# Performance work log

Measured on AMD Instinct MI355X. Metric: run time of the kernel, lower is better.

The kernel has to match this reference:

```python
import jax, jax.numpy as jnp
import numpy as np
from functools import partial

NP = 1024      # particles
T = 128        # timesteps
CUR_MIN, CUR_MAX = -2.0, 4.0
E_CRIT = 29000.0
F_STD = 0.005
G_STD = 0.01
NU = 1.0 / (G_STD * np.sqrt(2.0 * np.pi))

# VoC battery open-circuit-voltage curve constants
V_L, V_0 = -1.59614486, 4.13646328
GAMMA, ALPHA, BETA = 0.63726463, 1.40174122, 2.54478965


def voc(soc):
    return (V_L + (V_0 - V_L) * jnp.exp(GAMMA * (soc - 1.0))
            + ALPHA * V_L * (soc - 1.0)
            + (1.0 - ALPHA) * V_L * (jnp.exp(-BETA) - jnp.exp(-BETA * jnp.sqrt(soc))))


def setup_inputs() -> dict:
    key = jax.random.key(0)
    ks = jax.random.split(key, 11)
    soc_init = jax.random.uniform(ks[0], (NP, 1), jnp.float32, 0.3, 1.0)
    current = jax.random.normal(ks[1], (1, T), jnp.float32) * 0.5 + 1.0
    voltage_measured = 3.7 + 0.1 * jax.random.normal(ks[2], (1, T), jnp.float32)
    W1 = jax.random.normal(ks[3], (2, 1024), jnp.float32) / np.sqrt(2.0)
    b1 = jnp.zeros((1024,), jnp.float32)
    W2 = jax.random.normal(ks[4], (1024, 512), jnp.float32) / np.sqrt(1024.0)
    b2 = jnp.zeros((512,), jnp.float32)
    W3 = jax.random.normal(ks[5], (512, 1), jnp.float32) / np.sqrt(512.0)
    b3 = jnp.zeros((1,), jnp.float32)
    noise = jax.random.normal(ks[6], (T, NP, 1), jnp.float32)  # unit-std process noise
    u = jax.random.uniform(ks[7], (T,), jnp.float32)           # systematic-resampling offsets
    return {"soc_init": soc_init, "current": current, "voltage_measured": voltage_measured,
            "W1": W1, "b1": b1, "W2": W2, "b2": b2, "W3": W3, "b3": b3,
            "noise": noise, "u": u}


def _forward(soc_init, current, voltage_measured, W1, b1, W2, b2, W3, b3, noise, u):
    n = soc_init.shape[0]

    def mlp(x):  # [n,2] -> [n,1]
        z = jax.nn.sigmoid(x @ W1 + b1)
        z = jax.nn.sigmoid(z @ W2 + b2)
        return z @ W3 + b3

    def scale_I(I):
        return (I - CUR_MIN) / (CUR_MAX - CUR_MIN)

    cur = current[0]                       # [T]
    vmeas = voltage_measured[0]            # [T]
    cur_prev = jnp.concatenate([cur[:1], cur[:-1]])  # first step reuses current[0,0]

    def step(soc, xs):
        c_prev, c_t, vm, eps, ut = xs
        # --- prediction with previous current ---
        I = jnp.broadcast_to(c_prev, soc.shape)
        Z = mlp(jnp.concatenate([soc, scale_I(I)], axis=1))
        V = voc(soc) - I * Z
        soc = soc - I * V / E_CRIT + eps * F_STD
        soc = jnp.clip(soc, 1e-10, 1.0)
        # --- measurement update with current at t ---
        I = jnp.broadcast_to(c_t, soc.shape)
        sI = scale_I(I)
        Z = mlp(jnp.concatenate([soc, sI], axis=1))
        V = voc(soc) - I * Z
        logW = np.log(NU) - 0.5 * ((V - vm) / G_STD) ** 2  # [n,1]
        w = jnp.exp(logW - jnp.max(logW))[:, 0]
        wn = w / jnp.sum(w)
        # systematic resampling (deterministic given offset ut)
        cdf = jnp.cumsum(wn)
        pos = (ut + jnp.arange(n, dtype=jnp.float32)) / n
        idx = jnp.clip(jnp.searchsorted(cdf, pos), 0, n - 1)
        soc = soc[idx]
        # --- post-resample evaluation ---
        Z = mlp(jnp.concatenate([soc, sI], axis=1))
        V = voc(soc) - I * Z
        mse = jnp.mean((V - vm) ** 2)
        return soc, (mse, V[:, 0], soc[:, 0])

    soc0 = soc_init.astype(jnp.float32)
    _, (mses, Vs, socs) = jax.lax.scan(step, soc0, (cur_prev, cur, vmeas, noise, u))
    loss = jnp.mean(mses)        # == sum_t mse_t / T
    voltage = Vs.T               # [n, T]
    soc_hist = socs.T            # [n, T]
    return loss, voltage, soc_hist


def reference(soc_init, current, voltage_measured, W1, b1, W2, b2, W3, b3, noise, u):
    return _forward(soc_init, current, voltage_measured, W1, b1, W2, b2, W3, b3, noise, u)
```

## Files before the change

### kernel.cpp

```cpp
#include <hip/hip_runtime.h>
#include <stdint.h>

typedef __attribute__((ext_vector_type(8))) short short8;
typedef __attribute__((ext_vector_type(4))) float floatx4;

#define DONE_MAGIC 0x600DF00Du


__device__ __forceinline__ float sigm(float x) { return 1.0f / (1.0f + expf(-x)); }

__device__ __forceinline__ float vocf(float s) {
  const float V_L = -1.59614486f, V_0 = 4.13646328f;
  const float GAM = 0.63726463f, ALP = 1.40174122f, BET = 2.54478965f;
  return V_L + (V_0 - V_L) * expf(GAM * (s - 1.0f)) + ALP * V_L * (s - 1.0f)
       + (1.0f - ALP) * V_L * (expf(-BET) - expf(-BET * sqrtf(s)));
}

__device__ __forceinline__ unsigned short f2bf(float f) {
  unsigned u = __float_as_uint(f);
  u += 0x7FFFu + ((u >> 16) & 1u);
  return (unsigned short)(u >> 16);
}
__device__ __forceinline__ float bf2f(unsigned short b) {
  return __uint_as_float(((unsigned)b) << 16);
}

__device__ __forceinline__ float interp_c(const float* ctab, float s) {
  float f = s * 31.0f;
  float jf = fminf(floorf(f), 30.0f);
  int j = (int)jf;
  float u = f - jf;
  const float4 c = *(const float4*)&ctab[j * 4];
  return fmaf(fmaf(fmaf(c.w, u, c.z), u, c.y), u, c.x);
}

__device__ __forceinline__ int send_bl(float c, float u) {
  float C = c * 1024.0f;
  float sf = floorf(C - u);
  sf += (u + (sf + 1.0f) <= C) ? 1.0f : 0.0f;
  sf -= (u + sf > C) ? 1.0f : 0.0f;
  return (int)sf;
}

__device__ __forceinline__ float fast_exp2(float x) {
  float r;
  asm("v_exp_f32 %0, %1" : "=v"(r) : "v"(x));
  return r;
}


template<int C, int RM>
__device__ __forceinline__ float dpp_add_f(float x) {
  return __int_as_float(__builtin_amdgcn_update_dpp(0, __float_as_int(x), C, RM, 0xF, false));
}
template<int C, int RM>
__device__ __forceinline__ float dpp_old_f(float x) {
  return __int_as_float(__builtin_amdgcn_update_dpp(__float_as_int(x), __float_as_int(x), C, RM, 0xF, false));
}
template<int C, int RM>
__device__ __forceinline__ int dpp_old_i(int x) {
  return __builtin_amdgcn_update_dpp(x, x, C, RM, 0xF, false);
}
__device__ __forceinline__ float dpp_wshr1_f0(float x) {
  return __int_as_float(__builtin_amdgcn_update_dpp(0, __float_as_int(x), 0x138, 0xF, 0xF, true));
}
__device__ __forceinline__ int dpp_wshr1_i(int x, int old) {
  return __builtin_amdgcn_update_dpp(old, x, 0x138, 0xF, 0xF, false);
}
__device__ __forceinline__ int dpp_wshl1_i(int x, int old) {
  return __builtin_amdgcn_update_dpp(old, x, 0x130, 0xF, 0xF, false);
}

__device__ __forceinline__ float wave_iscan_add(float x) {
  x += dpp_add_f<0x111, 0xF>(x);
  x += dpp_add_f<0x112, 0xF>(x);
  x += dpp_add_f<0x114, 0xF>(x);
  x += dpp_add_f<0x118, 0xF>(x);
  x += dpp_add_f<0x142, 0xA>(x);
  x += dpp_add_f<0x143, 0xC>(x);
  return x;
}
__device__ __forceinline__ float wave_max_bcast(float x) {
  x = fmaxf(x, dpp_old_f<0xB1,  0xF>(x));
  x = fmaxf(x, dpp_old_f<0x4E,  0xF>(x));
  x = fmaxf(x, dpp_old_f<0x141, 0xF>(x));
  x = fmaxf(x, dpp_old_f<0x140, 0xF>(x));
  x = fmaxf(x, dpp_old_f<0x142, 0xA>(x));
  x = fmaxf(x, dpp_old_f<0x143, 0xC>(x));
  return __int_as_float(__builtin_amdgcn_readlane(__float_as_int(x), 63));
}
__device__ __forceinline__ int wave_iscan_max(int x) {
  x = max(x, dpp_old_i<0x111, 0xF>(x));
  x = max(x, dpp_old_i<0x112, 0xF>(x));
  x = max(x, dpp_old_i<0x114, 0xF>(x));
  x = max(x, dpp_old_i<0x118, 0xF>(x));
  x = max(x, dpp_old_i<0x142, 0xA>(x));
  x = max(x, dpp_old_i<0x143, 0xC>(x));
  return x;
}

__device__ __forceinline__ float rdlane_f(float x, int lane) {
  return __int_as_float(__builtin_amdgcn_readlane(__float_as_int(x), lane));
}

__device__ __forceinline__ void bar_lds() {
  asm volatile("s_waitcnt lgkmcnt(0)" ::: "memory");
  __builtin_amdgcn_s_barrier();
  asm volatile("" ::: "memory");
}


__global__ void __launch_bounds__(256)
k1_swizzle(const float* __restrict__ W2g, short* __restrict__ w2hiG, short* __restrict__ w2loG)
{
  int bid = blockIdx.x, tid = threadIdx.x;
  int pg = bid & 15, ng = bid >> 4;
  int u = pg * 256 + tid;
  int kb = u >> 7, l = u & 63, nt = (u >> 6) & 1, kq = l >> 4;
  int col = ng * 32 + nt * 16 + (l & 15);
  short8 hi8, lo8;
  #pragma unroll
  for (int j = 0; j < 8; j++) {
    int k = kb * 32 + kq * 8 + j;
    float w = W2g[k * 512 + col];
    unsigned short h = f2bf(w);
    hi8[j] = (short)h;
    lo8[j] = (short)f2bf(w - bf2f(h));
  }
  size_t off = ((size_t)ng * 4096 + u) * 8;
  *(short8*)(w2hiG + off) = hi8;
  *(short8*)(w2loG + off) = lo8;
}


__global__ void __launch_bounds__(256)
k2_gemm(const float* __restrict__ curg, const float* __restrict__ W1g,
        const float* __restrict__ b1g, const float* __restrict__ b2g,
        const float* __restrict__ W3g, const short* __restrict__ w2hiG,
        const short* __restrict__ w2loG, float* __restrict__ part)
{
  __shared__ short w2S[32768];
  __shared__ float b2S[32], w3S[32];

  const int tid = threadIdx.x, bid = blockIdx.x;
  const int ng = bid & 15, rtg = bid >> 4;
  const int wv = tid >> 6, ln = tid & 63;
  const int kq = ln >> 4;

  {
    const short* srcH = w2hiG + (size_t)ng * 32768;
    for (int i = tid; i < 4096; i += 256)
      *(short8*)(w2S + i * 8) = *(const short8*)(srcH + i * 8);
    if (tid < 32) { b2S[tid] = b2g[ng * 32 + tid]; w3S[tid] = W3g[ng * 32 + tid]; }
  }
  __syncthreads();

  const short* loG = w2loG + (size_t)ng * 32768;
  const int c = ln & 15, q = ln >> 4;
  const float b20 = b2S[c], b21 = b2S[16 + c];
  const float w30 = w3S[c], w31 = w3S[16 + c];

  for (int jj = 0; jj < 3; jj++) {
    int rt = rtg + 32 * jj;
    if (rt >= 72) break;
    int pt = rt * 4 + wv;
    unsigned r = pt * 16 + (ln & 15);
    unsigned t = r / 36u;
    int i = (int)(r - t * 36u);
    float soc = (float)(i - 1) * (1.0f / 31.0f);
    float sI = (curg[t] + 2.0f) / 6.0f;

    floatx4 acc0 = {0.f, 0.f, 0.f, 0.f};
    floatx4 acc1 = {0.f, 0.f, 0.f, 0.f};

    for (int kb = 0; kb < 32; kb++) {
      int k0 = kb * 32 + kq * 8;
      floatx4 wa0 = *(const floatx4*)(W1g + k0);
      floatx4 wa1 = *(const floatx4*)(W1g + k0 + 4);
      floatx4 wb0 = *(const floatx4*)(W1g + 1024 + k0);
      floatx4 wb1 = *(const floatx4*)(W1g + 1024 + k0 + 4);
      floatx4 bb0 = *(const floatx4*)(b1g + k0);
      floatx4 bb1 = *(const floatx4*)(b1g + k0 + 4);
      short8 ah, al;
      #pragma unroll
      for (int j = 0; j < 4; j++) {
        float x = soc * wa0[j] + sI * wb0[j] + bb0[j];
        float z = __builtin_amdgcn_rcpf(1.0f + __expf(-x));
        unsigned short h = f2bf(z);
        ah[j] = (short)h;
        al[j] = (short)f2bf(z - bf2f(h));
      }
      #pragma unroll
      for (int j = 0; j < 4; j++) {
        float x = soc * wa1[j] + sI * wb1[j] + bb1[j];
        float z = __builtin_amdgcn_rcpf(1.0f + __expf(-x));
        unsigned short h = f2bf(z);
        ah[4 + j] = (short)h;
        al[4 + j] = (short)f2bf(z - bf2f(h));
      }
      short8 bh0 = *(const short8*)(w2S + (kb * 2 + 0) * 512 + ln * 8);
      short8 bh1 = *(const short8*)(w2S + (kb * 2 + 1) * 512 + ln * 8);
      short8 bl0 = *(const short8*)(loG + (kb * 2 + 0) * 512 + ln * 8);
      short8 bl1 = *(const short8*)(loG + (kb * 2 + 1) * 512 + ln * 8);
      acc0 = __builtin_amdgcn_mfma_f32_16x16x32_bf16(ah, bh0, acc0, 0, 0, 0);
      acc1 = __builtin_amdgcn_mfma_f32_16x16x32_bf16(ah, bh1, acc1, 0, 0, 0);
      acc0 = __builtin_amdgcn_mfma_f32_16x16x32_bf16(ah, bl0, acc0, 0, 0, 0);
      acc1 = __builtin_amdgcn_mfma_f32_16x16x32_bf16(ah, bl1, acc1, 0, 0, 0);
      acc0 = __builtin_amdgcn_mfma_f32_16x16x32_bf16(al, bh0, acc0, 0, 0, 0);
      acc1 = __builtin_amdgcn_mfma_f32_16x16x32_bf16(al, bh1, acc1, 0, 0, 0);
    }

    #pragma unroll
    for (int r2 = 0; r2 < 4; r2++) {
      float v = w30 * sigm(acc0[r2] + b20) + w31 * sigm(acc1[r2] + b21);
      v += __shfl_xor(v, 1);
      v += __shfl_xor(v, 2);
      v += __shfl_xor(v, 4);
      v += __shfl_xor(v, 8);
      if (c == 0) part[(size_t)(pt * 16 + q * 4 + r2) * 16 + ng] = v;
    }
  }
}


__global__ void __launch_bounds__(256)
k3_table(const float* __restrict__ part, const float* __restrict__ b3g,
         const float* __restrict__ curg, float* __restrict__ VtabG)
{
  unsigned r = blockIdx.x * 256 + threadIdx.x;
  if (r < 4608) {
    const float* p = part + (size_t)r * 16;
    float s = 0.f;
    #pragma unroll
    for (int i = 0; i < 16; i++) s += p[i];
    float Z = s + b3g[0];
    unsigned t = r / 36u;
    int i = (int)(r - t * 36u);
    float node = (float)(i - 1) * (1.0f / 31.0f);
    float nodc = fmaxf(node, 1e-10f);
    VtabG[r] = vocf(nodc) - curg[t] * Z;
  }
}


__global__ void __launch_bounds__(256)
k3b_coeff(const float* __restrict__ VtabG, float* __restrict__ ctabG)
{
  int idx = blockIdx.x * 256 + threadIdx.x;
  if (idx < 3968) {
    int t = idx / 31, j = idx - t * 31;
    const float* nb = VtabG + t * 36 + j;
    float n0 = nb[0], n1 = nb[1], n2 = nb[2], n3 = nb[3];
    float c0 = n1;
    float c1 = (-2.0f * n0 - 3.0f * n1 + 6.0f * n2 - n3) * (1.0f / 6.0f);
    float c2 = (n0 - 2.0f * n1 + n2) * 0.5f;
    float c3 = (-n0 + 3.0f * (n1 - n2) + n3) * (1.0f / 6.0f);
    *(float4*)&ctabG[idx * 4] = make_float4(c0, c1, c2, c3);
  }
}


__device__ __forceinline__ int swzi(int j) { return ((j & 3) << 8) | (j >> 2); }

__global__ void __launch_bounds__(256)
pf_seq(const float* __restrict__ soc_init, const float* __restrict__ curg,
       const float* __restrict__ vmeasg, const float* __restrict__ noise_g,
       const float* __restrict__ u_g, const float* __restrict__ ctabG,
       float* __restrict__ vout, float* __restrict__ sout, float* __restrict__ outp,
       unsigned* __restrict__ flag)
{
  __shared__ float ctabS[15872];
  __shared__ float2 pvS[2][1024];
  __shared__ int   markS[1024] __attribute__((aligned(16)));
  __shared__ int   chunkS[4] __attribute__((aligned(16)));
  __shared__ float2 msS[4] __attribute__((aligned(16)));
  __shared__ float lossS[4];

  if (blockIdx.x != 0) {
    while (__hip_atomic_load(flag, __ATOMIC_RELAXED, __HIP_MEMORY_SCOPE_AGENT) != DONE_MAGIC) {
      __builtin_amdgcn_s_sleep(64);
    }
    return;
  }

  const int tid = threadIdx.x;
  const int w = tid >> 6, l = tid & 63;
  const int p0 = tid * 4;

  #pragma unroll
  for (int k = 0; k < 16; k++) {
    int i = tid + 256 * k;
    if (i < 3968) *(float4*)&ctabS[i * 4] = *(const float4*)&ctabG[i * 4];
  }
  float curA = curg[l],   curB = curg[64 + l];
  float vmA  = vmeasg[l], vmB  = vmeasg[64 + l];
  float uA   = u_g[l],    uB   = u_g[64 + l];
  *(int4*)&markS[p0] = make_int4(-1, -1, -1, -1);
  if (tid < 4) chunkS[tid] = -1;

  float sp0, sp1, sp2, sp3;
  {
    float4 s4 = *(const float4*)(soc_init + p0);
    float4 n4 = *(const float4*)(noise_g + p0);
    bar_lds();
    float c0 = rdlane_f(curA, 0);
    float c02 = c0 * (1.0f / 29000.0f);
    float spv[4];
    #pragma unroll
    for (int r = 0; r < 4; r++) {
      float si = ((const float*)&s4)[r];
      float V0 = interp_c(ctabS, si);
      float spn = fmaf(((const float*)&n4)[r], 0.005f, fmaf(-c02, V0, si));
      spv[r] = __builtin_amdgcn_fmed3f(spn, 1e-10f, 1.0f);
    }
    sp0 = spv[0]; sp1 = spv[1]; sp2 = spv[2]; sp3 = spv[3];
  }

  float lossAcc = 0.0f;

  for (int t = 0; t < 128; t++) {
    const float* ctab = ctabS + t * 124;
    const int cb = t & 1;
    float cI, vm, ut;
    if (t < 64) { cI = rdlane_f(curA, t); vm = rdlane_f(vmA, t); ut = rdlane_f(uA, t); }
    else        { cI = rdlane_f(curB, t - 64); vm = rdlane_f(vmB, t - 64); ut = rdlane_f(uB, t - 64); }
    float cI2 = cI * (1.0f / 29000.0f);

    int tn = (t < 127) ? t + 1 : 127;
    float4 noi4 = *(const float4*)(noise_g + tn * 1024 + p0);

    float V10 = interp_c(ctab, sp0);
    float V11 = interp_c(ctab, sp1);
    float V12 = interp_c(ctab, sp2);
    float V13 = interp_c(ctab, sp3);
    pvS[cb][tid]       = make_float2(sp0, V10);
    pvS[cb][256 + tid] = make_float2(sp1, V11);
    pvS[cb][512 + tid] = make_float2(sp2, V12);
    pvS[cb][768 + tid] = make_float2(sp3, V13);
    float d0 = V10 - vm, d1 = V11 - vm, d2 = V12 - vm, d3 = V13 - vm;
    float lw0 = d0 * d0 * -7213.4755594f;
    float lw1 = d1 * d1 * -7213.4755594f;
    float lw2 = d2 * d2 * -7213.4755594f;
    float lw3 = d3 * d3 * -7213.4755594f;

    float lmax = fmaxf(fmaxf(lw0, lw1), fmaxf(lw2, lw3));
    float mw = wave_max_bcast(lmax);
    float pr0, pr1, pr2, pr3, acc;
    {
      float w0 = fast_exp2(lw0 - mw); acc = w0;    pr0 = acc;
      float w1 = fast_exp2(lw1 - mw); acc += w1;   pr1 = acc;
      float w2 = fast_exp2(lw2 - mw); acc += w2;   pr2 = acc;
      float w3 = fast_exp2(lw3 - mw); acc += w3;   pr3 = acc;
    }
    float isc = wave_iscan_add(acc);
    if (l == 63) msS[w] = make_float2(mw, isc);
    bar_lds();

    float4 ms01 = *(const float4*)&msS[0];
    float4 ms23 = *(const float4*)&msS[2];
    float m = fmaxf(fmaxf(ms01.x, ms01.z), fmaxf(ms23.x, ms23.z));
    float f0 = fast_exp2(ms01.x - m), f1 = fast_exp2(ms01.z - m);
    float f2 = fast_exp2(ms23.x - m), f3 = fast_exp2(ms23.z - m);
    float t0 = ms01.y * f0, t1 = ms01.w * f1, t2 = ms23.y * f2, t3 = ms23.w * f3;
    float total = (t0 + t1) + (t2 + t3);
    float woff = (w > 0 ? t0 : 0.0f) + (w > 1 ? t1 : 0.0f) + (w > 2 ? t2 : 0.0f);
    float fw = (w == 0) ? f0 : ((w == 1) ? f1 : ((w == 2) ? f2 : f3));
    float exclw = dpp_wshr1_f0(isc);
    float rS = 1.0f / total;

    int se0 = send_bl(fmaf(exclw + pr0, fw, woff) * rS, ut);
    int se1 = send_bl(fmaf(exclw + pr1, fw, woff) * rS, ut);
    int se2 = send_bl(fmaf(exclw + pr2, fw, woff) * rS, ut);
    int se3 = send_bl(fmaf(exclw + pr3, fw, woff) * rS, ut);

    int nxt = dpp_wshl1_i(se0, se3);
    int tbase = t << 10;
    if (tid == 0 && se0 >= 0) { markS[0] = tbase; atomicMax(&chunkS[0], tbase); }
    if (se1 > se0 && se0 < 1023) {
      int s = se0 + 1, tg = tbase | (p0 + 1);
      markS[swzi(s)] = tg; atomicMax(&chunkS[s >> 8], tg);
    }
    if (se2 > se1 && se1 < 1023) {
      int s = se1 + 1, tg = tbase | (p0 + 2);
      markS[swzi(s)] = tg; atomicMax(&chunkS[s >> 8], tg);
    }
    if (se3 > se2 && se2 < 1023) {
      int s = se2 + 1, tg = tbase | (p0 + 3);
      markS[swzi(s)] = tg; atomicMax(&chunkS[s >> 8], tg);
    }
    if (l != 63) {
      if (nxt > se3 && se3 < 1023) {
        int s = se3 + 1, tg = tbase | (p0 + 4);
        markS[swzi(s)] = tg; atomicMax(&chunkS[s >> 8], tg);
      }
    } else {
      if (se3 < 1023) {
        int s = se3 + 1;
        int tg = (tid == 255) ? (tbase | 1023) : (tbase | (p0 + 4));
        atomicMax(&markS[swzi(s)], tg); atomicMax(&chunkS[s >> 8], tg);
      }
    }
    bar_lds();

    int mk0 = markS[tid],       mk1 = markS[256 + tid];
    int mk2 = markS[512 + tid], mk3 = markS[768 + tid];
    int4 ch4 = *(const int4*)chunkS;
    int q0 = mk0;
    int q1 = max(q0, mk1);
    int q2 = max(q1, mk2);
    int q3 = max(q2, mk3);
    int iscI = wave_iscan_max(q3);
    int ex = dpp_wshr1_i(iscI, -1);
    if (w > 0) ex = max(ex, ch4.x);
    if (w > 1) ex = max(ex, ch4.y);
    if (w > 2) ex = max(ex, ch4.z);

    int o0 = max(ex, q0) & 1023, o1 = max(ex, q1) & 1023;
    int o2 = max(ex, q2) & 1023, o3 = max(ex, q3) & 1023;
    float2 g0 = pvS[cb][swzi(o0)];
    float2 g1 = pvS[cb][swzi(o1)];
    float2 g2 = pvS[cb][swzi(o2)];
    float2 g3 = pvS[cb][swzi(o3)];

    *(float4*)(vout + t * 1024 + p0) = make_float4(g0.y, g1.y, g2.y, g3.y);
    *(float4*)(sout + t * 1024 + p0) = make_float4(g0.x, g1.x, g2.x, g3.x);

    float e0 = g0.y - vm, e1 = g1.y - vm, e2 = g2.y - vm, e3 = g3.y - vm;
    lossAcc = fmaf(e0, e0, lossAcc);
    lossAcc = fmaf(e1, e1, lossAcc);
    lossAcc = fmaf(e2, e2, lossAcc);
    lossAcc = fmaf(e3, e3, lossAcc);
    const float* nz = (const float*)&noi4;
    sp0 = __builtin_amdgcn_fmed3f(fmaf(nz[0], 0.005f, fmaf(-cI2, g0.y, g0.x)), 1e-10f, 1.0f);
    sp1 = __builtin_amdgcn_fmed3f(fmaf(nz[1], 0.005f, fmaf(-cI2, g1.y, g1.x)), 1e-10f, 1.0f);
    sp2 = __builtin_amdgcn_fmed3f(fmaf(nz[2], 0.005f, fmaf(-cI2, g2.y, g2.x)), 1e-10f, 1.0f);
    sp3 = __builtin_amdgcn_fmed3f(fmaf(nz[3], 0.005f, fmaf(-cI2, g3.y, g3.x)), 1e-10f, 1.0f);
  }

  float ls = wave_iscan_add(lossAcc);
  if (l == 63) lossS[w] = ls;
  bar_lds();
  if (tid == 0) {
    outp[0] = (lossS[0] + lossS[1] + lossS[2] + lossS[3]) * (1.0f / 131072.0f);
    __hip_atomic_store(flag, DONE_MAGIC, __ATOMIC_RELEASE, __HIP_MEMORY_SCOPE_AGENT);
  }
}


__global__ void __launch_bounds__(256)
k5_transpose(const float* __restrict__ vout, const float* __restrict__ sout,
             float* __restrict__ outp)
{
  __shared__ float tile[128 * 65];
  const int bid = blockIdx.x;
  const int arr = bid & 1;
  const int pg = bid >> 1;
  const float* src = arr ? sout : vout;
  float* dst = outp + 1 + arr * 131072;
  const int tid = threadIdx.x;
  const int p0 = pg * 64;

  #pragma unroll 4
  for (int s = 0; s < 32; s++) {
    int t = s * 4 + (tid >> 6);
    int p = tid & 63;
    tile[t * 65 + p] = src[t * 1024 + p0 + p];
  }
  __syncthreads();
  #pragma unroll 4
  for (int s = 0; s < 32; s++) {
    int pl = s * 2 + (tid >> 7);
    int t = tid & 127;
    dst[(p0 + pl) * 128 + t] = tile[t * 65 + pl];
  }
}


extern "C" void kernel_launch(void* const* d_in, const int* in_sizes, int n_in,
                              void* d_out, int out_size, void* d_ws, size_t ws_size,
                              hipStream_t stream) {
  const float* soc_init = (const float*)d_in[0];
  const float* cur      = (const float*)d_in[1];
  const float* vmeas    = (const float*)d_in[2];
  const float* W1       = (const float*)d_in[3];
  const float* b1       = (const float*)d_in[4];
  const float* W2       = (const float*)d_in[5];
  const float* b2       = (const float*)d_in[6];
  const float* W3       = (const float*)d_in[7];
  const float* b3       = (const float*)d_in[8];
  const float* noise    = (const float*)d_in[9];
  const float* u        = (const float*)d_in[10];
  float* out = (float*)d_out;
  char* ws = (char*)d_ws;

  short* w2hi   = (short*)ws;
  short* w2lo   = (short*)(ws + (1 << 20));
  float* part   = (float*)(ws + (2 << 20));
  char*  p3     = ws + (2 << 20) + 4608 * 16 * 4;
  float* VtabG  = (float*)p3;
  float* ctabG  = (float*)(p3 + 4608 * 4);
  float* vout   = (float*)(p3 + 4608 * 4 + 3968 * 16);
  float* sout   = (float*)(p3 + 4608 * 4 + 3968 * 16 + 1024 * 128 * 4);
  unsigned* flag = (unsigned*)(p3 + 4608 * 4 + 3968 * 16 + 2 * 1024 * 128 * 4);

  k1_swizzle<<<256, 256, 0, stream>>>(W2, w2hi, w2lo);
  k2_gemm<<<512, 256, 0, stream>>>(cur, W1, b1, b2, W3, w2hi, w2lo, part);
  k3_table<<<18, 256, 0, stream>>>(part, b3, cur, VtabG);
  k3b_coeff<<<16, 256, 0, stream>>>(VtabG, ctabG);
  pf_seq<<<256, 256, 0, stream>>>(soc_init, cur, vmeas, noise, u, ctabG, vout, sout, out, flag);
  k5_transpose<<<32, 256, 0, stream>>>(vout, sout, out);
}
```

Baseline: 325.4 us.

## Fuse spline-table build into pf_seq and write transposed outputs directly

The two small table kernels are folded into the particle-filter kernel. Each of its 128 blocks builds one timestep's cubic-coefficient row and publishes a per-block done flag, and block 0 spins on those flags before loading the table. The separate transpose kernel is also removed: block 0 now writes voltage and SOC histories straight into the final [n,T] layout. This cuts three kernel launches and an intermediate buffer round-trip, at the cost of strided, uncoalesced scalar stores inside the sequential timestep loop and a reliance on done flags that are never reset between calls.

```diff
diff --git a/kernel.cpp b/kernel.cpp
--- a/kernel.cpp
+++ b/kernel.cpp
@@ -223,50 +223,14 @@
 }
 
 
-__global__ void __launch_bounds__(256)
-k3_table(const float* __restrict__ part, const float* __restrict__ b3g,
-         const float* __restrict__ curg, float* __restrict__ VtabG)
-{
-  unsigned r = blockIdx.x * 256 + threadIdx.x;
-  if (r < 4608) {
-    const float* p = part + (size_t)r * 16;
-    float s = 0.f;
-    #pragma unroll
-    for (int i = 0; i < 16; i++) s += p[i];
-    float Z = s + b3g[0];
-    unsigned t = r / 36u;
-    int i = (int)(r - t * 36u);
-    float node = (float)(i - 1) * (1.0f / 31.0f);
-    float nodc = fmaxf(node, 1e-10f);
-    VtabG[r] = vocf(nodc) - curg[t] * Z;
-  }
-}
-
-
-__global__ void __launch_bounds__(256)
-k3b_coeff(const float* __restrict__ VtabG, float* __restrict__ ctabG)
-{
-  int idx = blockIdx.x * 256 + threadIdx.x;
-  if (idx < 3968) {
-    int t = idx / 31, j = idx - t * 31;
-    const float* nb = VtabG + t * 36 + j;
-    float n0 = nb[0], n1 = nb[1], n2 = nb[2], n3 = nb[3];
-    float c0 = n1;
-    float c1 = (-2.0f * n0 - 3.0f * n1 + 6.0f * n2 - n3) * (1.0f / 6.0f);
-    float c2 = (n0 - 2.0f * n1 + n2) * 0.5f;
-    float c3 = (-n0 + 3.0f * (n1 - n2) + n3) * (1.0f / 6.0f);
-    *(float4*)&ctabG[idx * 4] = make_float4(c0, c1, c2, c3);
-  }
-}
-
-
 __device__ __forceinline__ int swzi(int j) { return ((j & 3) << 8) | (j >> 2); }
 
 __global__ void __launch_bounds__(256)
 pf_seq(const float* __restrict__ soc_init, const float* __restrict__ curg,
        const float* __restrict__ vmeasg, const float* __restrict__ noise_g,
-       const float* __restrict__ u_g, const float* __restrict__ ctabG,
-       float* __restrict__ vout, float* __restrict__ sout, float* __restrict__ outp,
+       const float* __restrict__ u_g, const float* __restrict__ part,
+       const float* __restrict__ b3g, float* __restrict__ ctabG,
+       unsigned* __restrict__ doneG, float* __restrict__ outp,
        unsigned* __restrict__ flag)
 {
   __shared__ float ctabS[15872];
@@ -275,15 +239,50 @@
   __shared__ int   chunkS[4] __attribute__((aligned(16)));
   __shared__ float2 msS[4] __attribute__((aligned(16)));
   __shared__ float lossS[4];
-
-  if (blockIdx.x != 0) {
+  __shared__ float Vrow[36];
+
+  const int bid = blockIdx.x;
+  const int tid = threadIdx.x;
+
+  {
+    if (tid < 36) {
+      const float* p = part + (size_t)(bid * 36 + tid) * 16;
+      float s = 0.f;
+      #pragma unroll
+      for (int i = 0; i < 16; i++) s += p[i];
+      float Z = s + b3g[0];
+      float node = (float)(tid - 1) * (1.0f / 31.0f);
+      float nodc = fmaxf(node, 1e-10f);
+      Vrow[tid] = vocf(nodc) - curg[bid] * Z;
+    }
+    __syncthreads();
+    if (tid < 31) {
+      float n0 = Vrow[tid], n1 = Vrow[tid + 1], n2 = Vrow[tid + 2], n3 = Vrow[tid + 3];
+      float c0 = n1;
+      float c1 = (-2.0f * n0 - 3.0f * n1 + 6.0f * n2 - n3) * (1.0f / 6.0f);
+      float c2 = (n0 - 2.0f * n1 + n2) * 0.5f;
+      float c3 = (-n0 + 3.0f * (n1 - n2) + n3) * (1.0f / 6.0f);
+      *(float4*)&ctabG[(bid * 31 + tid) * 4] = make_float4(c0, c1, c2, c3);
+    }
+    __threadfence();
+    __syncthreads();
+    if (tid == 0)
+      __hip_atomic_store(&doneG[bid], DONE_MAGIC, __ATOMIC_RELEASE, __HIP_MEMORY_SCOPE_AGENT);
+  }
+
+  if (bid != 0) {
     while (__hip_atomic_load(flag, __ATOMIC_RELAXED, __HIP_MEMORY_SCOPE_AGENT) != DONE_MAGIC) {
       __builtin_amdgcn_s_sleep(64);
     }
     return;
   }
 
-  const int tid = threadIdx.x;
+  if (tid < 128) {
+    while (__hip_atomic_load(&doneG[tid], __ATOMIC_ACQUIRE, __HIP_MEMORY_SCOPE_AGENT) != DONE_MAGIC)
+      __builtin_amdgcn_s_sleep(1);
+  }
+  __syncthreads();
+
   const int w = tid >> 6, l = tid & 63;
   const int p0 = tid * 4;
 
@@ -317,6 +316,8 @@
   }
 
   float lossAcc = 0.0f;
+  float* vbase = outp + 1 + p0 * 128;
+  float* sbase = vbase + 131072;
 
   for (int t = 0; t < 128; t++) {
     const float* ctab = ctabS + t * 124;
@@ -422,8 +423,10 @@
     float2 g2 = pvS[cb][swzi(o2)];
     float2 g3 = pvS[cb][swzi(o3)];
 
-    *(float4*)(vout + t * 1024 + p0) = make_float4(g0.y, g1.y, g2.y, g3.y);
-    *(float4*)(sout + t * 1024 + p0) = make_float4(g0.x, g1.x, g2.x, g3.x);
+    vbase[t]       = g0.y;  sbase[t]       = g0.x;
+    vbase[128 + t] = g1.y;  sbase[128 + t] = g1.x;
+    vbase[256 + t] = g2.y;  sbase[256 + t] = g2.x;
+    vbase[384 + t] = g3.y;  sbase[384 + t] = g3.x;
 
     float e0 = g0.y - vm, e1 = g1.y - vm, e2 = g2.y - vm, e3 = g3.y - vm;
     lossAcc = fmaf(e0, e0, lossAcc);
@@ -443,35 +446,6 @@
   if (tid == 0) {
     outp[0] = (lossS[0] + lossS[1] + lossS[2] + lossS[3]) * (1.0f / 131072.0f);
     __hip_atomic_store(flag, DONE_MAGIC, __ATOMIC_RELEASE, __HIP_MEMORY_SCOPE_AGENT);
-  }
-}
-
-
-__global__ void __launch_bounds__(256)
-k5_transpose(const float* __restrict__ vout, const float* __restrict__ sout,
-             float* __restrict__ outp)
-{
-  __shared__ float tile[128 * 65];
-  const int bid = blockIdx.x;
-  const int arr = bid & 1;
-  const int pg = bid >> 1;
-  const float* src = arr ? sout : vout;
-  float* dst = outp + 1 + arr * 131072;
-  const int tid = threadIdx.x;
-  const int p0 = pg * 64;
-
-  #pragma unroll 4
-  for (int s = 0; s < 32; s++) {
-    int t = s * 4 + (tid >> 6);
-    int p = tid & 63;
-    tile[t * 65 + p] = src[t * 1024 + p0 + p];
-  }
-  __syncthreads();
-  #pragma unroll 4
-  for (int s = 0; s < 32; s++) {
-    int pl = s * 2 + (tid >> 7);
-    int t = tid & 127;
-    dst[(p0 + pl) * 128 + t] = tile[t * 65 + pl];
   }
 }
 
@@ -493,20 +467,16 @@
   float* out = (float*)d_out;
   char* ws = (char*)d_ws;
 
-  short* w2hi   = (short*)ws;
-  short* w2lo   = (short*)(ws + (1 << 20));
-  float* part   = (float*)(ws + (2 << 20));
-  char*  p3     = ws + (2 << 20) + 4608 * 16 * 4;
-  float* VtabG  = (float*)p3;
-  float* ctabG  = (float*)(p3 + 4608 * 4);
-  float* vout   = (float*)(p3 + 4608 * 4 + 3968 * 16);
-  float* sout   = (float*)(p3 + 4608 * 4 + 3968 * 16 + 1024 * 128 * 4);
-  unsigned* flag = (unsigned*)(p3 + 4608 * 4 + 3968 * 16 + 2 * 1024 * 128 * 4);
+  short* w2hi    = (short*)ws;
+  short* w2lo    = (short*)(ws + (1 << 20));
+  float* part    = (float*)(ws + (2 << 20));
+  char*  p3      = ws + (2 << 20) + 4608 * 16 * 4;
+  float* ctabG   = (float*)p3;
+  unsigned* doneG = (unsigned*)(p3 + 3968 * 16);
+  unsigned* flag  = (unsigned*)(p3 + 3968 * 16 + 512);
 
   k1_swizzle<<<256, 256, 0, stream>>>(W2, w2hi, w2lo);
   k2_gemm<<<512, 256, 0, stream>>>(cur, W1, b1, b2, W3, w2hi, w2lo, part);
-  k3_table<<<18, 256, 0, stream>>>(part, b3, cur, VtabG);
-  k3b_coeff<<<16, 256, 0, stream>>>(VtabG, ctabG);
-  pf_seq<<<256, 256, 0, stream>>>(soc_init, cur, vmeas, noise, u, ctabG, vout, sout, out, flag);
-  k5_transpose<<<32, 256, 0, stream>>>(vout, sout, out);
-}
+  pf_seq<<<128, 256, 0, stream>>>(soc_init, cur, vmeas, noise, u, part, b3,
+                                  ctabG, doneG, out, flag);
+}
```

Result: slower. 383.4 us (+17.8%).
